# Optimization experiments

Hardware: AMD Instinct MI355X
Metric: run time of the kernel (lower is better)

The kernel has to match this reference:

```python
import jax, jax.numpy as jnp
import numpy as np

B, S, E, H, L, D, G, V = 32, 256, 300, 256, 4000, 256, 512, 50000
LIN1, LIN2 = 512, 256  # linear_size


def _glorot(key, shape):
    fan_in, fan_out = shape[-1], shape[-2] if len(shape) > 1 else shape[-1]
    std = np.sqrt(2.0 / (fan_in + fan_out))
    return jax.random.normal(key, shape, dtype=jnp.float32) * std


def setup_inputs() -> dict:
    key = jax.random.key(0)
    ks = jax.random.split(key, 20)
    tokens = jax.random.randint(ks[0], (B, S), 1, V)  # avoid padding_idx=0
    emb_table = jax.random.normal(ks[1], (V, E), dtype=jnp.float32) * 0.1
    emb_table = emb_table.at[0].set(0.0)  # padding row
    # bidirectional LSTM (1 layer), torch gate order i,f,g,o
    w_ih_f = _glorot(ks[2], (4 * H, E));  w_hh_f = _glorot(ks[3], (4 * H, H))
    b_f = jnp.zeros((4 * H,), jnp.float32)
    w_ih_b = _glorot(ks[4], (4 * H, E));  w_hh_b = _glorot(ks[5], (4 * H, H))
    b_b = jnp.zeros((4 * H,), jnp.float32)
    # MLAttention: Linear(2H -> L, bias=False)
    attn_w = _glorot(ks[6], (L, 2 * H))
    # label graph branch
    label_emb = _glorot(ks[7], (L, D))
    adj_raw = (jax.random.uniform(ks[8], (L, L)) < 0.004).astype(jnp.float32)
    adj_raw = adj_raw + jnp.eye(L, dtype=jnp.float32)
    deg = jnp.sum(adj_raw, axis=1, keepdims=True)
    adj = adj_raw / deg  # row-normalized dense adjacency [L, L]
    gcn_w = _glorot(ks[9], (D, G));  gcn_b = jnp.zeros((G,), jnp.float32)
    # MLLinear([2H+G, 512, 256], 1)
    w1 = _glorot(ks[10], (2 * H + G, LIN1));  b1 = jnp.zeros((LIN1,), jnp.float32)
    w2 = _glorot(ks[11], (LIN1, LIN2));       b2 = jnp.zeros((LIN2,), jnp.float32)
    w_out = _glorot(ks[12], (LIN2, 1));       b_out = jnp.zeros((1,), jnp.float32)
    return dict(tokens=tokens, emb_table=emb_table,
                w_ih_f=w_ih_f, w_hh_f=w_hh_f, b_f=b_f,
                w_ih_b=w_ih_b, w_hh_b=w_hh_b, b_b=b_b,
                attn_w=attn_w, label_emb=label_emb, adj=adj,
                gcn_w=gcn_w, gcn_b=gcn_b,
                w1=w1, b1=b1, w2=w2, b2=b2, w_out=w_out, b_out=b_out)


def _lstm_dir(x_gates, w_hh, reverse):
    # x_gates: [B, S, 4H] precomputed input projections (+bias)
    def step(carry, xt):
        h, c = carry
        gates = xt + h @ w_hh.T
        i, f, g, o = jnp.split(gates, 4, axis=-1)
        c = jax.nn.sigmoid(f) * c + jax.nn.sigmoid(i) * jnp.tanh(g)
        h = jax.nn.sigmoid(o) * jnp.tanh(c)
        return (h, c), h
    b = x_gates.shape[0]
    init = (jnp.zeros((b, H), x_gates.dtype), jnp.zeros((b, H), x_gates.dtype))
    _, hs = jax.lax.scan(step, init, jnp.swapaxes(x_gates, 0, 1), reverse=reverse)
    return jnp.swapaxes(hs, 0, 1)  # [B, S, H]


def reference(tokens, emb_table, w_ih_f, w_hh_f, b_f, w_ih_b, w_hh_b, b_b,
              attn_w, label_emb, adj, gcn_w, gcn_b,
              w1, b1, w2, b2, w_out, b_out):
    masks = tokens != 0  # [B, S]
    emb_out = emb_table[tokens]  # [B, S, E]
    # bidirectional LSTM -> [B, S, 2H]
    gates_f = jnp.einsum('bse,ge->bsg', emb_out, w_ih_f) + b_f
    gates_b = jnp.einsum('bse,ge->bsg', emb_out, w_ih_b) + b_b
    rnn_out = jnp.concatenate([_lstm_dir(gates_f, w_hh_f, False),
                               _lstm_dir(gates_b, w_hh_b, True)], axis=-1)
    # MLAttention: per-label attention over sequence
    scores = jnp.einsum('bsh,lh->bls', rnn_out, attn_w)  # [B, L, S]
    scores = jnp.where(masks[:, None, :], scores, jnp.float32(-1e9))
    attn = jax.nn.softmax(scores, axis=-1)
    attn_out = jnp.einsum('bls,bsh->blh', attn, rnn_out)  # [B, L, 2H]
    # GCN over label graph: relu(A @ (X W) + b), single layer [D -> G]
    gcn_out = jax.nn.relu(adj @ (label_emb @ gcn_w) + gcn_b)  # [L, G]
    gcn_out = jnp.broadcast_to(gcn_out[None], (attn_out.shape[0], L, G))
    # concat fusion + MLLinear([2H+G, 512, 256], 1)
    x = jnp.concatenate([attn_out, gcn_out], axis=-1)  # [B, L, 2H+G]
    x = jax.nn.relu(x @ w1 + b1)
    x = jax.nn.relu(x @ w2 + b2)
    out = jnp.squeeze(x @ w_out + b_out, -1)  # [B, L]
    return out
```

## Files before the change

### kernel.cpp

```cpp
#include <hip/hip_runtime.h>
#include <hip/hip_bf16.h>
#include <math.h>


typedef __attribute__((ext_vector_type(8))) short bfrag;
typedef __attribute__((ext_vector_type(4))) float ffrag;

__device__ __forceinline__ ushort f2bf(float x) {
    union { float f; unsigned u; } c; c.f = x;
    const unsigned r = c.u + 0x7fffu + ((c.u >> 16) & 1u);
    return (ushort)(r >> 16);
}
__device__ __forceinline__ float bf2f(ushort h) {
    union { unsigned u; float f; } c; c.u = (unsigned)h << 16;
    return c.f;
}

template<bool BIAS, bool ADDROW, bool RELU, bool OUTF, bool OUTS>
__global__ __launch_bounds__(256) void mgemm_k(
    const ushort* __restrict__ A, const ushort* __restrict__ B,
    float* __restrict__ Cf, ushort* __restrict__ Cs,
    int M, int N, int K, int lda, int ldb, int ldc, int ldcs,
    long abs_, long bbs_, long cbs_, long csbs_,
    const float* __restrict__ bias,
    const float* __restrict__ addrow, int addmod, int ldadd)
{
    const int tid = threadIdx.x;
    const int ln = tid & 63;
    const int wv = tid >> 6;
    const int wm = wv >> 1, wn = wv & 1;
    const int m0 = blockIdx.x * 128, n0 = blockIdx.y * 128;
    const int z = blockIdx.z;
    A += (size_t)z * abs_;
    B += (size_t)z * bbs_;

    __shared__ ushort Ah[128 * 40], Al[128 * 40], Bh[128 * 40], Bl[128 * 40];

    ffrag acc[4][4];
#pragma unroll
    for (int i = 0; i < 4; ++i)
#pragma unroll
        for (int j = 0; j < 4; ++j) acc[i][j] = ffrag{0.f, 0.f, 0.f, 0.f};

    const int sr = tid >> 1;
    const int sk = (tid & 1) * 16;
    const int am = min(m0 + sr, M - 1);
    const int bn = n0 + sr;
    const int fr = ln & 15;
    const int fk = (ln >> 4) * 8;

    const ushort* arow = A + (size_t)am * lda + sk;
    const ushort* brow = B + (size_t)bn * ldb + sk;

    bfrag ah0, ah1, al0, al1, bh0, bh1, bl0, bl1;
    {
        const ushort* ap = arow;
        const ushort* bp = brow;
        ah0 = *(const bfrag*)ap;       ah1 = *(const bfrag*)(ap + 8);
        al0 = *(const bfrag*)(ap + K); al1 = *(const bfrag*)(ap + K + 8);
        bh0 = *(const bfrag*)bp;       bh1 = *(const bfrag*)(bp + 8);
        bl0 = *(const bfrag*)(bp + K); bl1 = *(const bfrag*)(bp + K + 8);
    }

    for (int k0 = 0; k0 < K; k0 += 32) {
        __syncthreads();
        *(bfrag*)&Ah[sr * 40 + sk] = ah0;  *(bfrag*)&Ah[sr * 40 + sk + 8] = ah1;
        *(bfrag*)&Al[sr * 40 + sk] = al0;  *(bfrag*)&Al[sr * 40 + sk + 8] = al1;
        *(bfrag*)&Bh[sr * 40 + sk] = bh0;  *(bfrag*)&Bh[sr * 40 + sk + 8] = bh1;
        *(bfrag*)&Bl[sr * 40 + sk] = bl0;  *(bfrag*)&Bl[sr * 40 + sk + 8] = bl1;
        __syncthreads();
        if (k0 + 32 < K) {
            const ushort* ap = arow + k0 + 32;
            const ushort* bp = brow + k0 + 32;
            ah0 = *(const bfrag*)ap;       ah1 = *(const bfrag*)(ap + 8);
            al0 = *(const bfrag*)(ap + K); al1 = *(const bfrag*)(ap + K + 8);
            bh0 = *(const bfrag*)bp;       bh1 = *(const bfrag*)(bp + 8);
            bl0 = *(const bfrag*)(bp + K); bl1 = *(const bfrag*)(bp + K + 8);
        }
        bfrag afh[4], afl[4];
#pragma unroll
        for (int i = 0; i < 4; ++i) {
            const int ar = (wm * 64 + i * 16 + fr) * 40 + fk;
            afh[i] = *(const bfrag*)&Ah[ar];
            afl[i] = *(const bfrag*)&Al[ar];
        }
#pragma unroll
        for (int j = 0; j < 4; ++j) {
            const int br = (wn * 64 + j * 16 + fr) * 40 + fk;
            const bfrag bfh = *(const bfrag*)&Bh[br];
            const bfrag bfl = *(const bfrag*)&Bl[br];
#pragma unroll
            for (int i = 0; i < 4; ++i) {
                acc[i][j] = __builtin_amdgcn_mfma_f32_16x16x32_bf16(afh[i], bfh, acc[i][j], 0, 0, 0);
                acc[i][j] = __builtin_amdgcn_mfma_f32_16x16x32_bf16(afh[i], bfl, acc[i][j], 0, 0, 0);
                acc[i][j] = __builtin_amdgcn_mfma_f32_16x16x32_bf16(afl[i], bfh, acc[i][j], 0, 0, 0);
            }
        }
    }

#pragma unroll
    for (int i = 0; i < 4; ++i) {
#pragma unroll
        for (int rg = 0; rg < 4; ++rg) {
            const int gm = m0 + wm * 64 + i * 16 + (ln >> 4) * 4 + rg;
            if (gm >= M) continue;
            const float* addp = ADDROW ? (addrow + (size_t)(gm % addmod) * ldadd) : nullptr;
#pragma unroll
            for (int j = 0; j < 4; ++j) {
                const int gn = n0 + wn * 64 + j * 16 + fr;
                float v = acc[i][j][rg];
                if (BIAS) v += bias[gn];
                if (ADDROW) v += addp[gn];
                if (RELU) v = fmaxf(v, 0.f);
                if (OUTF) Cf[(size_t)z * cbs_ + (size_t)gm * ldc + gn] = v;
                if (OUTS) {
                    const ushort h = f2bf(v);
                    const ushort l = f2bf(v - bf2f(h));
                    ushort* cp = Cs + (size_t)z * csbs_ + (size_t)gm * ldcs;
                    cp[gn] = h;
                    cp[N + gn] = l;
                }
            }
        }
    }
}

__global__ void gsplit_k(const float* __restrict__ src, const int* __restrict__ tok,
                         ushort* __restrict__ outp, int K, int Kpad)
{
    const int r = blockIdx.x;
    const float* s = src + (size_t)(tok ? tok[r] : r) * K;
    ushort* o = outp + (size_t)r * 2 * Kpad;
    for (int k = threadIdx.x; k < Kpad; k += blockDim.x) {
        const float x = (k < K) ? s[k] : 0.f;
        const ushort h = f2bf(x);
        const ushort l = f2bf(x - bf2f(h));
        o[k] = h;
        o[Kpad + k] = l;
    }
}

__global__ void split_k(const float* __restrict__ in, ushort* __restrict__ outp,
                        int rows, int K)
{
    const int i = blockIdx.x * 256 + threadIdx.x;
    if (i >= rows * K) return;
    const int r = i / K, k = i - r * K;
    const float x = in[i];
    const ushort h = f2bf(x);
    const ushort l = f2bf(x - bf2f(h));
    ushort* o = outp + (size_t)r * 2 * K;
    o[k] = h;
    o[K + k] = l;
}

__global__ __launch_bounds__(256) void tsplit_k(
    const float* __restrict__ in, ushort* __restrict__ outp,
    int R, int C, int ldin, long ibs, long obs)
{
    __shared__ float t[64][65];
    const int c0 = blockIdx.x * 64, r0 = blockIdx.y * 64;
    in   += (size_t)blockIdx.z * ibs;
    outp += (size_t)blockIdx.z * obs;
    const int tx = threadIdx.x & 15, ty = threadIdx.x >> 4;
#pragma unroll
    for (int i = 0; i < 4; ++i) {
        const int r = ty * 4 + i;
        const float4 v = *(const float4*)&in[(size_t)(r0 + r) * ldin + c0 + tx * 4];
        t[tx * 4 + 0][r] = v.x;
        t[tx * 4 + 1][r] = v.y;
        t[tx * 4 + 2][r] = v.z;
        t[tx * 4 + 3][r] = v.w;
    }
    __syncthreads();
    const int R2 = 2 * R;
#pragma unroll
    for (int i = 0; i < 4; ++i) {
        const int c = ty * 4 + i;
        ushort h[4], l[4];
#pragma unroll
        for (int k2 = 0; k2 < 4; ++k2) {
            const float x = t[c][tx * 4 + k2];
            h[k2] = f2bf(x);
            l[k2] = f2bf(x - bf2f(h[k2]));
        }
        uint2 hw, lw;
        hw.x = (unsigned)h[0] | ((unsigned)h[1] << 16);
        hw.y = (unsigned)h[2] | ((unsigned)h[3] << 16);
        lw.x = (unsigned)l[0] | ((unsigned)l[1] << 16);
        lw.y = (unsigned)l[2] | ((unsigned)l[3] << 16);
        *(uint2*)&outp[(size_t)(c0 + c) * R2 + r0 + tx * 4] = hw;
        *(uint2*)&outp[(size_t)(c0 + c) * R2 + R + r0 + tx * 4] = lw;
    }
}

__global__ __launch_bounds__(1024) void lstm_reg_k(
    const float* __restrict__ gxf, const float* __restrict__ gxb,
    const float* __restrict__ whf, const float* __restrict__ whb,
    float* __restrict__ rnn, unsigned long long* hbuf)
{
    const int p = blockIdx.x;
    const int q = blockIdx.y;
    const int b = p >> 1, dir = p & 1;
    const float* xg = dir ? gxb : gxf;
    const float* W  = dir ? whb : whf;
    const int tid = threadIdx.x;
    const int wv = tid >> 6, lane = tid & 63;
    const int ul = lane >> 4;
    const int ks = (lane >> 2) & 3;
    const int gt = lane & 3;
    const int u  = wv * 4 + ul;
    const int grow = gt * 256 + q * 64 + u;

    float4 w[16];
    {
        const float4* wp = (const float4*)(W + (size_t)grow * 256 + ks * 64);
#pragma unroll
        for (int i = 0; i < 16; ++i) w[i] = wp[i];
    }

    __shared__ float h_lds[4 * 68];
    __shared__ float xg_lds[320];

    unsigned long long* hb0 = hbuf + (size_t)p * 256;
    unsigned long long* hb1 = hbuf + (size_t)(64 + p) * 256;

    const size_t xgb = (size_t)b * 256;
    const int g2 = (tid >> 6) * 256 + q * 64 + (tid & 63);
    float c = 0.f;
    float xg_cur = 0.f;
    if (tid < 256) xg_cur = xg[(xgb + (dir ? 255 : 0)) * 1024 + g2];

    for (int st = 0; st < 256; ++st) {
        const int ts = dir ? 255 - st : st;
        if (tid < 256) {
            float hv = 0.f;
            if (st > 0) {
                unsigned long long* src = (st & 1) ? hb0 : hb1;
                unsigned long long wd;
                do {
                    wd = __hip_atomic_load(&src[tid], __ATOMIC_RELAXED, __HIP_MEMORY_SCOPE_AGENT);
                } while ((unsigned)(wd >> 32) != (unsigned)st);
                union { unsigned uu; float f; } cv; cv.uu = (unsigned)wd;
                hv = cv.f;
            }
            h_lds[(tid >> 6) * 68 + (tid & 63)] = hv;
            xg_lds[(tid & 63) * 5 + (tid >> 6)] = xg_cur;
        }
        __syncthreads();
        float acc = 0.f;
        {
            const float4* hp = (const float4*)&h_lds[ks * 68];
#pragma unroll
            for (int i = 0; i < 16; ++i) {
                const float4 hv = hp[i];
                acc = fmaf(w[i].x, hv.x, acc);
                acc = fmaf(w[i].y, hv.y, acc);
                acc = fmaf(w[i].z, hv.z, acc);
                acc = fmaf(w[i].w, hv.w, acc);
            }
        }
        acc += __shfl_xor(acc, 4);
        acc += __shfl_xor(acc, 8);
        const float g = acc + xg_lds[u * 5 + gt];
        __syncthreads();
        const float t1 = __shfl_xor(g, 1);
        const float t2 = __shfl_xor(g, 2);
        const float t3 = __shfl_xor(t1, 2);
        const float g0 = (gt == 0) ? g : (gt == 1) ? t1 : (gt == 2) ? t2 : t3;
        const float g1 = (gt == 1) ? g : (gt == 0) ? t1 : (gt == 3) ? t2 : t3;
        const float g2v = (gt == 2) ? g : (gt == 3) ? t1 : (gt == 0) ? t2 : t3;
        const float g3v = (gt == 3) ? g : (gt == 2) ? t1 : (gt == 1) ? t2 : t3;
        const float si = 1.f / (1.f + __expf(-g0));
        const float sf = 1.f / (1.f + __expf(-g1));
        const float so = 1.f / (1.f + __expf(-g3v));
        const float tg = 1.f - 2.f / (__expf(2.f * g2v) + 1.f);
        c = sf * c + si * tg;
        const float tc = 1.f - 2.f / (__expf(2.f * c) + 1.f);
        const float hn = so * tc;
        if ((lane & 15) == 0) {
            unsigned long long* dst = (st & 1) ? hb1 : hb0;
            union { float f; unsigned uu; } hv2; hv2.f = hn;
            const unsigned long long wd =
                ((unsigned long long)(unsigned)(st + 1) << 32) | (unsigned long long)hv2.uu;
            __hip_atomic_store(&dst[q * 64 + u], wd, __ATOMIC_RELAXED, __HIP_MEMORY_SCOPE_AGENT);
            rnn[(xgb + ts) * 512 + (size_t)dir * 256 + q * 64 + u] = hn;
        }
        if (tid < 256 && st < 255) {
            const int tsn = dir ? 254 - st : st + 1;
            xg_cur = xg[(xgb + tsn) * 1024 + g2];
        }
    }
}

__global__ void init_hbuf_k(unsigned long long* hbuf) {
    const int i = blockIdx.x * 256 + threadIdx.x;
    if (i < 32768) hbuf[i] = 0ull;
}

__global__ __launch_bounds__(256) void softmax_split_k(
    float* __restrict__ sc, const int* __restrict__ tokens, int b0)
{
    const int bb = blockIdx.y;
    const int l  = blockIdx.x * 4 + (threadIdx.x >> 6);
    const int lane = threadIdx.x & 63;
    float* row = sc + ((size_t)bb * 4000 + l) * 256;
    const int* tk = tokens + (size_t)(b0 + bb) * 256;
    float4 v = *(const float4*)&row[lane * 4];
    const int4 tv = *(const int4*)&tk[lane * 4];
    if (tv.x == 0) v.x = -1e9f;
    if (tv.y == 0) v.y = -1e9f;
    if (tv.z == 0) v.z = -1e9f;
    if (tv.w == 0) v.w = -1e9f;
    float mx = fmaxf(fmaxf(v.x, v.y), fmaxf(v.z, v.w));
    for (int o = 32; o > 0; o >>= 1) mx = fmaxf(mx, __shfl_xor(mx, o));
    v.x = __expf(v.x - mx); v.y = __expf(v.y - mx);
    v.z = __expf(v.z - mx); v.w = __expf(v.w - mx);
    float s = v.x + v.y + v.z + v.w;
    for (int o = 32; o > 0; o >>= 1) s += __shfl_xor(s, o);
    const float inv = 1.f / s;
    const float p0 = v.x * inv, p1 = v.y * inv, p2 = v.z * inv, p3 = v.w * inv;
    const ushort h0 = f2bf(p0), h1 = f2bf(p1), h2 = f2bf(p2), h3 = f2bf(p3);
    const ushort l0 = f2bf(p0 - bf2f(h0)), l1 = f2bf(p1 - bf2f(h1));
    const ushort l2 = f2bf(p2 - bf2f(h2)), l3 = f2bf(p3 - bf2f(h3));
    ushort* orow = (ushort*)row;
    uint2 hw, lw;
    hw.x = (unsigned)h0 | ((unsigned)h1 << 16);
    hw.y = (unsigned)h2 | ((unsigned)h3 << 16);
    lw.x = (unsigned)l0 | ((unsigned)l1 << 16);
    lw.y = (unsigned)l2 | ((unsigned)l3 << 16);
    *(uint2*)&orow[lane * 4] = hw;
    *(uint2*)&orow[256 + lane * 4] = lw;
}

__global__ __launch_bounds__(256) void spmm_k(
    const float* __restrict__ adj, const float* __restrict__ tmp,
    const float* __restrict__ bias, float* __restrict__ outp)
{
    const int l = blockIdx.x;
    __shared__ int   idxs[4][256];
    __shared__ float vals[4][256];
    __shared__ int   cnts[4];
    const int t = threadIdx.x;
    const int w = t >> 6, lane = t & 63;
    const float* arow = adj + (size_t)l * 4000;
    int cnt = 0;
    for (int r = 0; r < 16; ++r) {
        const int o = r * 64 + lane;
        const int j = w * 1000 + o;
        const float a = (o < 1000) ? arow[j] : 0.f;
        const unsigned long long mk = __ballot(a != 0.f);
        if (a != 0.f) {
            const int pos = cnt + __popcll(mk & ((1ull << lane) - 1ull));
            if (pos < 256) { idxs[w][pos] = j; vals[w][pos] = a; }
        }
        cnt += __popcll(mk);
    }
    if (lane == 0) cnts[w] = min(cnt, 256);
    __syncthreads();
    const int c0 = t * 2;
    float a0 = 0.f, a1 = 0.f;
    for (int ww = 0; ww < 4; ++ww) {
        const int n = cnts[ww];
        for (int e = 0; e < n; ++e) {
            const float a = vals[ww][e];
            const float2 tv = *(const float2*)&tmp[(size_t)idxs[ww][e] * 512 + c0];
            a0 = fmaf(a, tv.x, a0);
            a1 = fmaf(a, tv.y, a1);
        }
    }
    float2 res;
    res.x = fmaxf(a0 + bias[c0], 0.f);
    res.y = fmaxf(a1 + bias[c0 + 1], 0.f);
    *(float2*)&outp[(size_t)l * 512 + c0] = res;
}

__global__ __launch_bounds__(256) void out_k(
    const float* __restrict__ x2, const float* __restrict__ w_out,
    const float* __restrict__ b_out, float* __restrict__ outp, int b0)
{
    const int r = blockIdx.x * 4 + (threadIdx.x >> 6);
    const int lane = threadIdx.x & 63;
    const float4 xv = *(const float4*)&x2[(size_t)r * 256 + lane * 4];
    const float4 wv = *(const float4*)&w_out[lane * 4];
    float s = xv.x * wv.x + xv.y * wv.y + xv.z * wv.z + xv.w * wv.w;
    for (int o = 32; o > 0; o >>= 1) s += __shfl_xor(s, o);
    if (lane == 0) {
        const int bb = r / 4000, l = r - bb * 4000;
        outp[(size_t)(b0 + bb) * 4000 + l] = s + b_out[0];
    }
}

extern "C" void kernel_launch(void* const* d_in, const int* in_sizes, int n_in,
                              void* d_out, int out_size, void* d_ws, size_t ws_size,
                              hipStream_t stream)
{
    const int*   tokens    = (const int*)  d_in[0];
    const float* emb       = (const float*)d_in[1];
    const float* w_ih_f    = (const float*)d_in[2];
    const float* w_hh_f    = (const float*)d_in[3];
    const float* b_f       = (const float*)d_in[4];
    const float* w_ih_b    = (const float*)d_in[5];
    const float* w_hh_b    = (const float*)d_in[6];
    const float* b_b       = (const float*)d_in[7];
    const float* attn_w    = (const float*)d_in[8];
    const float* label_emb = (const float*)d_in[9];
    const float* adj       = (const float*)d_in[10];
    const float* gcn_w     = (const float*)d_in[11];
    const float* gcn_b     = (const float*)d_in[12];
    const float* w1        = (const float*)d_in[13];
    const float* b1        = (const float*)d_in[14];
    const float* w2        = (const float*)d_in[15];
    const float* b2        = (const float*)d_in[16];
    const float* w_out     = (const float*)d_in[17];
    const float* b_out     = (const float*)d_in[18];
    float* outp = (float*)d_out;
    float* wsf  = (float*)d_ws;

    const size_t off_gf  = 0;
    const size_t off_gb  = 8388608;
    const size_t off_rnn = 16777216;
    const size_t off_tmp = 20971520;
    const size_t off_go  = 23019520;
    const size_t off_ctr = 25067520;
    const size_t base_end = 27115520;
    const size_t S_sz = 10829824;
    const size_t have = ws_size / 4;
    int NB = 1; size_t offS = off_gf, offC = off_gf + S_sz;
    {
        const int tiers[6] = {32, 16, 8, 4, 2, 0};
        bool found = false;
        for (int t = 0; tiers[t]; ++t) {
            if (have >= base_end + S_sz + (size_t)tiers[t] * 5120000) {
                NB = tiers[t]; offS = base_end; offC = base_end + S_sz; found = true; break;
            }
        }
        if (!found && have >= base_end + S_sz) { NB = 2; offS = base_end; offC = off_gf; }
    }

    float* gates_f = wsf + off_gf;
    float* gates_b = wsf + off_gb;
    float* rnn     = wsf + off_rnn;
    float* gcn_tmp = wsf + off_tmp;
    float* gcn_out = wsf + off_go;
    float* contrib = wsf + off_ctr;
    unsigned long long* hbuf = (unsigned long long*)(wsf + off_tmp);

    const size_t off_esp = (offS == off_gf) ? off_rnn : offS;
    ushort* esplit  = (ushort*)(wsf + off_esp);
    ushort* wsplitf = esplit + (size_t)8192 * 640;
    ushort* wsplitb = wsplitf + (size_t)1024 * 640;

    ushort* attn_ws16 = (ushort*)(wsf + offS);
    ushort* w1t16     = (ushort*)(wsf + offS + 2048000);
    ushort* w2t16     = (ushort*)(wsf + offS + 2310144);
    ushort* rnn_nt16  = (ushort*)(wsf + offS + 2441216);
    ushort* rnnT16    = (ushort*)(wsf + offS + 6635520);

    float*  scoresb = wsf + offC;
    ushort* attn16  = (ushort*)(wsf + offC + (size_t)NB * 1024000);
    ushort* x116    = (ushort*)(wsf + offC + (size_t)NB * 1024000 + (size_t)NB * 2048000);
    float*  x2b     = scoresb;

    ushort* le16   = (ushort*)(wsf + offC);
    ushort* gw16   = le16 + (size_t)4000 * 512;
    ushort* go16   = gw16 + (size_t)512 * 512;
    ushort* w1b16  = go16 + (size_t)4000 * 1024;

    init_hbuf_k<<<128, 256, 0, stream>>>(hbuf);

    gsplit_k<<<8192, 256, 0, stream>>>(emb, tokens, esplit, 300, 320);
    gsplit_k<<<1024, 256, 0, stream>>>(w_ih_f, nullptr, wsplitf, 300, 320);
    gsplit_k<<<1024, 256, 0, stream>>>(w_ih_b, nullptr, wsplitb, 300, 320);
    mgemm_k<true, false, false, true, false><<<dim3(64, 8, 1), 256, 0, stream>>>(
        esplit, wsplitf, gates_f, nullptr,
        8192, 1024, 320, 640, 640, 1024, 0,
        0L, 0L, 0L, 0L, b_f, nullptr, 1, 0);
    mgemm_k<true, false, false, true, false><<<dim3(64, 8, 1), 256, 0, stream>>>(
        esplit, wsplitb, gates_b, nullptr,
        8192, 1024, 320, 640, 640, 1024, 0,
        0L, 0L, 0L, 0L, b_b, nullptr, 1, 0);

    lstm_reg_k<<<dim3(64, 4), 1024, 0, stream>>>(
        gates_f, gates_b, w_hh_f, w_hh_b, rnn, hbuf);

    split_k<<<16384, 256, 0, stream>>>(rnn, rnn_nt16, 8192, 512);
    tsplit_k<<<dim3(8, 4, 32), 256, 0, stream>>>(rnn, rnnT16, 256, 512, 512, 131072, 262144);
    split_k<<<8000, 256, 0, stream>>>(attn_w, attn_ws16, 4000, 512);
    tsplit_k<<<dim3(8, 8, 1), 256, 0, stream>>>(w1, w1t16, 512, 512, 512, 0, 0);
    tsplit_k<<<dim3(4, 8, 1), 256, 0, stream>>>(w2, w2t16, 512, 256, 256, 0, 0);

    split_k<<<4000, 256, 0, stream>>>(label_emb, le16, 4000, 256);
    tsplit_k<<<dim3(8, 4, 1), 256, 0, stream>>>(gcn_w, gw16, 256, 512, 512, 0, 0);
    mgemm_k<false, false, false, true, false><<<dim3(32, 4, 1), 256, 0, stream>>>(
        le16, gw16, gcn_tmp, nullptr,
        4000, 512, 256, 512, 512, 512, 0,
        0L, 0L, 0L, 0L, nullptr, nullptr, 1, 0);
    spmm_k<<<dim3(4000), 256, 0, stream>>>(adj, gcn_tmp, gcn_b, gcn_out);
    split_k<<<8000, 256, 0, stream>>>(gcn_out, go16, 4000, 512);
    tsplit_k<<<dim3(8, 8, 1), 256, 0, stream>>>(w1 + (size_t)512 * 512, w1b16, 512, 512, 512, 0, 0);
    mgemm_k<true, false, false, true, false><<<dim3(32, 4, 1), 256, 0, stream>>>(
        go16, w1b16, contrib, nullptr,
        4000, 512, 512, 1024, 1024, 512, 0,
        0L, 0L, 0L, 0L, b1, nullptr, 1, 0);

    for (int b0 = 0; b0 < 32; b0 += NB) {
        const int nb = (32 - b0 < NB) ? (32 - b0) : NB;
        mgemm_k<false, false, false, true, false><<<dim3(32, 2, nb), 256, 0, stream>>>(
            attn_ws16, rnn_nt16 + (size_t)b0 * 262144, scoresb, nullptr,
            4000, 256, 512, 1024, 1024, 256, 0,
            0L, 262144L, 1024000L, 0L, nullptr, nullptr, 1, 0);
        softmax_split_k<<<dim3(1000, nb), 256, 0, stream>>>(scoresb, tokens, b0);
        mgemm_k<false, false, false, false, true><<<dim3(32, 4, nb), 256, 0, stream>>>(
            (const ushort*)scoresb, rnnT16 + (size_t)b0 * 262144, nullptr, attn16,
            4000, 512, 256, 512, 512, 0, 1024,
            2048000L, 262144L, 0L, 4096000L, nullptr, nullptr, 1, 0);
        mgemm_k<false, true, true, false, true><<<dim3((nb * 4000 + 127) / 128, 4, 1), 256, 0, stream>>>(
            attn16, w1t16, nullptr, x116,
            nb * 4000, 512, 512, 1024, 1024, 0, 1024,
            0L, 0L, 0L, 0L, nullptr, contrib, 4000, 512);
        mgemm_k<true, false, true, true, false><<<dim3((nb * 4000 + 127) / 128, 2, 1), 256, 0, stream>>>(
            x116, w2t16, x2b, nullptr,
            nb * 4000, 256, 512, 1024, 1024, 256, 0,
            0L, 0L, 0L, 0L, b2, nullptr, 1, 0);
        out_k<<<dim3(nb * 1000), 256, 0, stream>>>(x2b, w_out, b_out, outp, b0);
    }
}
```

Baseline: 1.745 ms.

## Replace per-element tagged h polling with per-block step counters in LSTM

The cross-workgroup hand-off of the hidden state in the persistent LSTM kernel changes. Before, each of 256 threads spun on its own 64-bit word that packed a step tag with the value. Now one thread per block polls four per-block int stamps, followed by a block barrier and plain 32-bit reads of h. This is meant to cut polling traffic and the 64-bit atomics on the serial recurrence critical path. In exchange it adds a barrier and a stamp store per step, and it relies on relaxed atomics with no explicit release/acquire fence, so the h values could in principle be read before they are visible.

```diff
diff --git a/kernel.cpp b/kernel.cpp
--- a/kernel.cpp
+++ b/kernel.cpp
@@ -197,7 +197,7 @@
 __global__ __launch_bounds__(1024) void lstm_reg_k(
     const float* __restrict__ gxf, const float* __restrict__ gxb,
     const float* __restrict__ whf, const float* __restrict__ whb,
-    float* __restrict__ rnn, unsigned long long* hbuf)
+    float* __restrict__ rnn, float* hbuf, int* stamp)
 {
     const int p = blockIdx.x;
     const int q = blockIdx.y;
@@ -222,8 +222,9 @@
     __shared__ float h_lds[4 * 68];
     __shared__ float xg_lds[320];
 
-    unsigned long long* hb0 = hbuf + (size_t)p * 256;
-    unsigned long long* hb1 = hbuf + (size_t)(64 + p) * 256;
+    float* hb0 = hbuf + (size_t)p * 256;
+    float* hb1 = hbuf + (size_t)(64 + p) * 256;
+    int* sp = stamp + p * 16;
 
     const size_t xgb = (size_t)b * 256;
     const int g2 = (tid >> 6) * 256 + q * 64 + (tid & 63);
@@ -233,16 +234,21 @@
 
     for (int st = 0; st < 256; ++st) {
         const int ts = dir ? 255 - st : st;
+        if (st > 0 && tid == 0) {
+            while (true) {
+                int s0 = __hip_atomic_load(&sp[0], __ATOMIC_RELAXED, __HIP_MEMORY_SCOPE_AGENT);
+                int s1 = __hip_atomic_load(&sp[1], __ATOMIC_RELAXED, __HIP_MEMORY_SCOPE_AGENT);
+                int s2 = __hip_atomic_load(&sp[2], __ATOMIC_RELAXED, __HIP_MEMORY_SCOPE_AGENT);
+                int s3 = __hip_atomic_load(&sp[3], __ATOMIC_RELAXED, __HIP_MEMORY_SCOPE_AGENT);
+                if (min(min(s0, s1), min(s2, s3)) >= st) break;
+            }
+        }
+        __syncthreads();
         if (tid < 256) {
             float hv = 0.f;
             if (st > 0) {
-                unsigned long long* src = (st & 1) ? hb0 : hb1;
-                unsigned long long wd;
-                do {
-                    wd = __hip_atomic_load(&src[tid], __ATOMIC_RELAXED, __HIP_MEMORY_SCOPE_AGENT);
-                } while ((unsigned)(wd >> 32) != (unsigned)st);
-                union { unsigned uu; float f; } cv; cv.uu = (unsigned)wd;
-                hv = cv.f;
+                const float* src = (st & 1) ? hb0 : hb1;
+                hv = __hip_atomic_load(&src[tid], __ATOMIC_RELAXED, __HIP_MEMORY_SCOPE_AGENT);
             }
             h_lds[(tid >> 6) * 68 + (tid & 63)] = hv;
             xg_lds[(tid & 63) * 5 + (tid >> 6)] = xg_cur;
@@ -263,7 +269,6 @@
         acc += __shfl_xor(acc, 4);
         acc += __shfl_xor(acc, 8);
         const float g = acc + xg_lds[u * 5 + gt];
-        __syncthreads();
         const float t1 = __shfl_xor(g, 1);
         const float t2 = __shfl_xor(g, 2);
         const float t3 = __shfl_xor(t1, 2);
@@ -279,12 +284,13 @@
         const float tc = 1.f - 2.f / (__expf(2.f * c) + 1.f);
         const float hn = so * tc;
         if ((lane & 15) == 0) {
-            unsigned long long* dst = (st & 1) ? hb1 : hb0;
-            union { float f; unsigned uu; } hv2; hv2.f = hn;
-            const unsigned long long wd =
-                ((unsigned long long)(unsigned)(st + 1) << 32) | (unsigned long long)hv2.uu;
-            __hip_atomic_store(&dst[q * 64 + u], wd, __ATOMIC_RELAXED, __HIP_MEMORY_SCOPE_AGENT);
+            float* dst = (st & 1) ? hb1 : hb0;
+            __hip_atomic_store(&dst[q * 64 + u], hn, __ATOMIC_RELAXED, __HIP_MEMORY_SCOPE_AGENT);
             rnn[(xgb + ts) * 512 + (size_t)dir * 256 + q * 64 + u] = hn;
+        }
+        __syncthreads();
+        if (tid == 0) {
+            __hip_atomic_store(&sp[q], st + 1, __ATOMIC_RELAXED, __HIP_MEMORY_SCOPE_AGENT);
         }
         if (tid < 256 && st < 255) {
             const int tsn = dir ? 254 - st : st + 1;
@@ -293,9 +299,9 @@
     }
 }
 
-__global__ void init_hbuf_k(unsigned long long* hbuf) {
-    const int i = blockIdx.x * 256 + threadIdx.x;
-    if (i < 32768) hbuf[i] = 0ull;
+__global__ void init_cnt_k(int* stamp) {
+    const int i = blockIdx.x * blockDim.x + threadIdx.x;
+    if (i < 1024) stamp[i] = 0;
 }
 
 __global__ __launch_bounds__(256) void softmax_split_k(
@@ -444,7 +450,8 @@
     float* gcn_tmp = wsf + off_tmp;
     float* gcn_out = wsf + off_go;
     float* contrib = wsf + off_ctr;
-    unsigned long long* hbuf = (unsigned long long*)(wsf + off_tmp);
+    float* hbuf    = wsf + off_tmp;
+    int*   stamp   = (int*)(wsf + off_tmp + 32768);
 
     const size_t off_esp = (offS == off_gf) ? off_rnn : offS;
     ushort* esplit  = (ushort*)(wsf + off_esp);
@@ -467,7 +474,7 @@
     ushort* go16   = gw16 + (size_t)512 * 512;
     ushort* w1b16  = go16 + (size_t)4000 * 1024;
 
-    init_hbuf_k<<<128, 256, 0, stream>>>(hbuf);
+    init_cnt_k<<<4, 256, 0, stream>>>(stamp);
 
     gsplit_k<<<8192, 256, 0, stream>>>(emb, tokens, esplit, 300, 320);
     gsplit_k<<<1024, 256, 0, stream>>>(w_ih_f, nullptr, wsplitf, 300, 320);
@@ -482,7 +489,7 @@
         0L, 0L, 0L, 0L, b_b, nullptr, 1, 0);
 
     lstm_reg_k<<<dim3(64, 4), 1024, 0, stream>>>(
-        gates_f, gates_b, w_hh_f, w_hh_b, rnn, hbuf);
+        gates_f, gates_b, w_hh_f, w_hh_b, rnn, hbuf, stamp);
 
     split_k<<<16384, 256, 0, stream>>>(rnn, rnn_nt16, 8192, 512);
     tsplit_k<<<dim3(8, 4, 32), 256, 0, stream>>>(rnn, rnnT16, 256, 512, 512, 131072, 262144);
```

Measured after the change: 1.770 ms. No clear change (+1.4%).
